# Performance work log

Measured on AMD Instinct MI355X. Metric: run time of the kernel, lower is better.

The kernel has to match this reference:

```python
import jax, jax.numpy as jnp
import numpy as np

EMBED_DIM = 1024
NUM_HEADS = 16
HEAD_DIM = EMBED_DIM // NUM_HEADS


def setup_inputs() -> dict:
    key = jax.random.key(0)
    ks = jax.random.split(key, 9)
    B, S, D = 2, 2048, EMBED_DIM
    scale = 1.0 / np.sqrt(D)
    x = jax.random.normal(ks[0], (B, S, D), dtype=jnp.float32)
    # Linear params (torch nn.Linear: y = x @ W.T + b); store W as [out, in]
    Wq = jax.random.normal(ks[1], (D, D), dtype=jnp.float32) * scale
    bq = jnp.zeros((D,), dtype=jnp.float32)
    Wk = jax.random.normal(ks[2], (D, D), dtype=jnp.float32) * scale
    bk = jnp.zeros((D,), dtype=jnp.float32)
    Wv = jax.random.normal(ks[3], (D, D), dtype=jnp.float32) * scale
    bv = jnp.zeros((D,), dtype=jnp.float32)
    Wo = jax.random.normal(ks[4], (D, D), dtype=jnp.float32) * scale
    bo = jnp.zeros((D,), dtype=jnp.float32)
    return {"x": x, "Wq": Wq, "bq": bq, "Wk": Wk, "bk": bk,
            "Wv": Wv, "bv": bv, "Wo": Wo, "bo": bo}


def reference(x, Wq, bq, Wk, bk, Wv, bv, Wo, bo):
    B, S, D = x.shape
    H, Hd = NUM_HEADS, HEAD_DIM
    scaling = Hd ** -0.5
    # projections (torch Linear: x @ W.T + b)
    q = (x @ Wq.T + bq).reshape(B, S, H, Hd).transpose(0, 2, 1, 3)  # [B,H,S,Hd]
    k = (x @ Wk.T + bk).reshape(B, S, H, Hd).transpose(0, 2, 1, 3)
    v = (x @ Wv.T + bv).reshape(B, S, H, Hd).transpose(0, 2, 1, 3)
    # full score matrix, as in the original (no flash tiling)
    scores = jnp.einsum('bhqd,bhkd->bhqk', q, k) * scaling  # [B,H,S,S]
    attn = jax.nn.softmax(scores, axis=-1)
    # dropout is identity in eval mode
    out = jnp.einsum('bhqk,bhkd->bhqd', attn, v)  # [B,H,S,Hd]
    out = out.transpose(0, 2, 1, 3).reshape(B, S, D)
    return out @ Wo.T + bo
```

## Files before the change

### kernel.cpp

```cpp
#include <hip/hip_runtime.h>
#include <stdint.h>

typedef unsigned short u16;
typedef short short8 __attribute__((ext_vector_type(8)));
typedef float f32x4 __attribute__((ext_vector_type(4)));

__device__ __forceinline__ u16 f2bf_fast(float f) {
  union { float f; uint32_t u; } x;
  x.f = f;
  return (u16)((x.u + 0x8000u) >> 16);
}

__device__ __forceinline__ uint32_t pack2bf(float lo, float hi) {
  union { float f; uint32_t u; } a, b;
  a.f = lo; b.f = hi;
  return __builtin_amdgcn_perm(b.u + 0x8000u, a.u + 0x8000u, 0x07060302u);
}

__device__ __forceinline__ float bf2f(uint32_t u) {
  union { uint32_t u; float f; } x;
  x.u = u << 16;
  return x.f;
}

__device__ __forceinline__ void gload_lds16(const void* g, void* l) {
  __builtin_amdgcn_global_load_lds(
      (const __attribute__((address_space(1))) void*)g,
      (__attribute__((address_space(3))) void*)l, 16, 0, 0);
}

__device__ __forceinline__ f32x4 mfma16(short8 a, short8 b, f32x4 c) {
  return __builtin_amdgcn_mfma_f32_16x16x32_bf16(a, b, c, 0, 0, 0);
}

__device__ __forceinline__ short8 ldfrag(const u16* base, int tile, int kc,
                                         int lane) {
  return *(const short8*)(base + ((((tile << 5) + kc) << 6) + lane) * 8);
}

#define QSCALE 0.18033688011112042f

__global__ void pack_all(const float* __restrict__ x, const float* __restrict__ wq,
                         const float* __restrict__ wk, const float* __restrict__ wv,
                         const float* __restrict__ wo, u16* __restrict__ xp,
                         u16* __restrict__ wp) {
  const int gi = blockIdx.x * 256 + threadIdx.x;
  const int lane = gi & 63;
  const int kc = (gi >> 6) & 31;
  const int rt = gi >> 11;
  const int col = kc * 32 + (lane >> 4) * 8;
  const float* src;
  int row;
  if (rt < 256) {
    src = x;
    row = rt * 16 + (lane & 15);
  } else {
    const int wti = rt - 256;
    const int widx = wti >> 6;
    src = (widx == 0) ? wq : (widx == 1) ? wk : (widx == 2) ? wv : wo;
    row = (wti & 63) * 16 + (lane & 15);
  }
  const float4* p = (const float4*)(src + (size_t)row * 1024 + col);
  const float4 v0 = p[0], v1 = p[1];
  uint4 o;
  o.x = pack2bf(v0.x, v0.y);
  o.y = pack2bf(v0.z, v0.w);
  o.z = pack2bf(v1.x, v1.y);
  o.w = pack2bf(v1.z, v1.w);
  u16* dst = (rt < 256) ? xp : wp;
  const int og = (rt < 256) ? gi : gi - 524288;
  ((uint4*)dst)[og] = o;
}

__global__ __launch_bounds__(256, 3) void proj_qkv(
    const u16* __restrict__ xp, const u16* __restrict__ wp,
    const float* __restrict__ bq, const float* __restrict__ bk,
    const float* __restrict__ bv, u16* __restrict__ qw, u16* __restrict__ kw,
    u16* __restrict__ vw) {
  const int wv2 = threadIdx.x >> 6;
  const int lane = threadIdx.x & 63;
  const int quad = lane >> 4, l15 = lane & 15;
  const int xcd = blockIdx.x & 7;
  const int bidx = blockIdx.x >> 3;
  const int xq = xcd >> 1, xh = xcd & 1;
  const bool isQK = bidx < 64;
  int at0, bt0, bm, bn;
  const u16 *Ap, *Bp;
  if (isQK) {
    const int q = bidx;
    bn = xh * 16 + (q & 15);
    bm = xq * 16 + (q >> 4) * 4 + wv2;
    Ap = xp; at0 = bm * 4;
    Bp = wp; bt0 = bn * 4;
  } else {
    const int v = bidx - 64;
    bn = xq * 16 + (v & 15);
    bm = xh * 8 + (v >> 4) * 4 + wv2;
    Ap = wp; at0 = 128 + bm * 4;
    Bp = xp; bt0 = bn * 4;
  }

  f32x4 acc[4][4] = {};
  short8 af[2][4], bf[2][4];
#pragma unroll
  for (int mt = 0; mt < 4; ++mt) af[0][mt] = ldfrag(Ap, at0 + mt, 0, lane);
#pragma unroll
  for (int nt = 0; nt < 4; ++nt) bf[0][nt] = ldfrag(Bp, bt0 + nt, 0, lane);

#pragma unroll 4
  for (int kc = 0; kc < 32; ++kc) {
    const int cur = kc & 1, nxt = cur ^ 1;
    if (kc < 31) {
#pragma unroll
      for (int mt = 0; mt < 4; ++mt)
        af[nxt][mt] = ldfrag(Ap, at0 + mt, kc + 1, lane);
#pragma unroll
      for (int nt = 0; nt < 4; ++nt)
        bf[nxt][nt] = ldfrag(Bp, bt0 + nt, kc + 1, lane);
    }
#pragma unroll
    for (int mt = 0; mt < 4; ++mt)
#pragma unroll
      for (int nt = 0; nt < 4; ++nt)
        acc[mt][nt] = mfma16(af[cur][mt], bf[cur][nt], acc[mt][nt]);
  }

#pragma unroll
  for (int nt = 0; nt < 4; ++nt) {
    const int n = bn * 64 + nt * 16 + l15;
#pragma unroll
    for (int mt = 0; mt < 4; ++mt)
#pragma unroll
      for (int r = 0; r < 4; ++r) {
        const int m = bm * 64 + mt * 16 + quad * 4 + r;
        const float a = acc[mt][nt][r];
        if (isQK) {
          const bool isQ = (bn < 16);
          const int nn = isQ ? n : n - 1024;
          const float v = isQ ? (a + bq[nn]) * QSCALE : a + bk[nn];
          u16* op = isQ ? qw : kw;
          const int b = m >> 11, s = m & 2047, hh = nn >> 6, d = nn & 63;
          op[((size_t)((b * 16 + hh) * 2048 + s)) * 64 + d] = f2bf_fast(v);
        } else {
          const float v = a + bv[m];
          const int b = n >> 11, s = n & 2047;
          vw[((size_t)(b * 1024 + m)) * 2048 + s] = f2bf_fast(v);
        }
      }
  }
}

__global__ __launch_bounds__(256) void attn_kernel(
    const u16* __restrict__ Q, const u16* __restrict__ Kt,
    const u16* __restrict__ Vt, u16* __restrict__ op0, u16* __restrict__ op1,
    float* __restrict__ lp) {
  __shared__ __align__(16) u16 Sm[16384];
  const int tid = threadIdx.x, lane = tid & 63, w = tid >> 6;
  const int quad = lane >> 4, l15 = lane & 15;
  const int qt = blockIdx.x;
  const int bh = blockIdx.y >> 1;
  const int ks = blockIdx.y & 1;
  const int sl = (l15 & 3) | ((l15 >> 1) & 4) | ((l15 << 1) & 8);

  const char* Qb = (const char*)(Q + ((size_t)bh * 2048 + qt * 128) * 64);
  const char* Kb = (const char*)(Kt + ((size_t)bh * 2048 + ks * 1024) * 64);
  const char* Vb = (const char*)(Vt + (size_t)bh * 64 * 2048 + ks * 1024);

  auto stageKV = [&](int kt, int b) {
    u16* Kl = Sm + b * 4096;
    u16* Vl = Sm + 8192 + b * 4096;
#pragma unroll
    for (int i = 0; i < 2; ++i) {
      const int G = (w * 2 + i) * 64 + lane;
      const int r = G >> 3, slw = G & 7;
      gload_lds16(Kb + (size_t)(kt * 64 + r) * 128 + ((slw ^ (r & 7)) * 16),
                  &Kl[G * 8]);
      gload_lds16(Vb + (size_t)r * 4096 + kt * 128 + ((slw ^ (r & 7)) * 16),
                  &Vl[G * 8]);
    }
  };

#pragma unroll
  for (int i = 0; i < 4; ++i) {
    const int G = (w * 4 + i) * 64 + lane;
    const int row = G >> 3, slw = G & 7;
    u16* qdst = (G < 512) ? (Sm + 4096) : (Sm + 12288);
    gload_lds16(Qb + (size_t)row * 128 + ((slw ^ (row & 7)) * 16),
                &qdst[(G & 511) * 8]);
  }
  stageKV(0, 0);
  __syncthreads();

  const u16* qreg = (w < 2) ? (Sm + 4096) : (Sm + 12288);
  const int qr0 = (w & 1) * 32;
  short8 aq[2][2];
#pragma unroll
  for (int mt = 0; mt < 2; ++mt)
#pragma unroll
    for (int kc = 0; kc < 2; ++kc)
      aq[mt][kc] = *(const short8*)&qreg[(qr0 + mt * 16 + l15) * 64 +
                                         (((kc * 4 + quad) ^ (l15 & 7)) * 8)];
  __syncthreads();

  f32x4 ot[4][2] = {};
  float lsum[2] = {};

  for (int kt = 0; kt < 16; ++kt) {
    const int buf = kt & 1;
    if (kt < 15) stageKV(kt + 1, buf ^ 1);
    const u16* Kl = Sm + buf * 4096;
    const u16* Vl = Sm + 8192 + buf * 4096;

    f32x4 st[2][4] = {};
#pragma unroll
    for (int kc = 0; kc < 2; ++kc)
#pragma unroll
      for (int ntk = 0; ntk < 4; ++ntk) {
        short8 kf = *(const short8*)&Kl[(ntk * 16 + sl) * 64 +
                                        (((kc * 4 + quad) ^ (sl & 7)) * 8)];
        st[0][ntk] = mfma16(kf, aq[0][kc], st[0][ntk]);
        st[1][ntk] = mfma16(kf, aq[1][kc], st[1][ntk]);
      }

    uint2 pp[2][4];
#pragma unroll
    for (int mt = 0; mt < 2; ++mt)
#pragma unroll
      for (int ntk = 0; ntk < 4; ++ntk) {
        const float e0 = __builtin_amdgcn_exp2f(st[mt][ntk][0]);
        const float e1 = __builtin_amdgcn_exp2f(st[mt][ntk][1]);
        const float e2 = __builtin_amdgcn_exp2f(st[mt][ntk][2]);
        const float e3 = __builtin_amdgcn_exp2f(st[mt][ntk][3]);
        lsum[mt] += (e0 + e1) + (e2 + e3);
        pp[mt][ntk].x = pack2bf(e0, e1);
        pp[mt][ntk].y = pack2bf(e2, e3);
      }

    short8 pf[2][2];
#pragma unroll
    for (int mt = 0; mt < 2; ++mt)
#pragma unroll
      for (int g = 0; g < 2; ++g) {
        const uint2 o0 = pp[mt][2 * g], o1 = pp[mt][2 * g + 1];
        const uint32_t x0l = __shfl_xor(o0.x, 32), x0h = __shfl_xor(o0.y, 32);
        const uint32_t x1l = __shfl_xor(o1.x, 32), x1h = __shfl_xor(o1.y, 32);
        union { uint32_t u[4]; short8 s; } f;
        if (quad < 2) {
          f.u[0] = o0.x; f.u[1] = o0.y; f.u[2] = x0l; f.u[3] = x0h;
        } else {
          f.u[0] = x1l; f.u[1] = x1h; f.u[2] = o1.x; f.u[3] = o1.y;
        }
        pf[mt][g] = f.s;
      }

#pragma unroll
    for (int g = 0; g < 2; ++g)
#pragma unroll
      for (int ntd = 0; ntd < 4; ++ntd) {
        short8 vf = *(const short8*)&Vl[(ntd * 16 + l15) * 64 +
                                        (((g * 4 + quad) ^ (l15 & 7)) * 8)];
        ot[ntd][0] = mfma16(vf, pf[0][g], ot[ntd][0]);
        ot[ntd][1] = mfma16(vf, pf[1][g], ot[ntd][1]);
      }
    if (kt < 15) __syncthreads();
  }

  const int b = bh >> 4, h = bh & 15;
  u16* op = ks ? op1 : op0;
#pragma unroll
  for (int mt = 0; mt < 2; ++mt) {
    float l = lsum[mt];
    l += __shfl_xor(l, 16);
    l += __shfl_xor(l, 32);
    const int srow = qt * 128 + w * 32 + mt * 16 + l15;
    if (quad == 0) lp[((size_t)(ks * 32 + bh)) * 2048 + srow] = l;
    const int rt = b * 128 + qt * 8 + w * 2 + mt;
#pragma unroll
    for (int ntd = 0; ntd < 4; ++ntd) {
      const int kc = h * 2 + (ntd >> 1);
      const int lnq = ((ntd & 1) * 2 + (quad >> 1)) & 3;
      const int j0 = (quad & 1) * 4;
      uint2 ov;
      ov.x = pack2bf(ot[ntd][mt][0], ot[ntd][mt][1]);
      ov.y = pack2bf(ot[ntd][mt][2], ot[ntd][mt][3]);
      *(uint2*)(op + ((size_t)((rt * 32 + kc) * 64 + lnq * 16 + l15)) * 8 + j0) = ov;
    }
  }
}

__global__ void attn_combine(const u16* __restrict__ op0,
                             const u16* __restrict__ op1,
                             const float* __restrict__ lp,
                             u16* __restrict__ awp) {
  const int g = blockIdx.x * 256 + threadIdx.x;
  const int ln = g & 63;
  const int kc = (g >> 6) & 31;
  const int rt = g >> 11;
  const int row = rt * 16 + (ln & 15);
  const int b = row >> 11, s = row & 2047;
  const int h = kc >> 1;
  const int lidx = (b * 16 + h) * 2048 + s;
  const float inv = __builtin_amdgcn_rcpf(lp[lidx] + lp[lidx + 65536]);
  const uint4 a0 = ((const uint4*)op0)[g];
  const uint4 a1 = ((const uint4*)op1)[g];
  uint4 o;
  o.x = pack2bf((bf2f(a0.x) + bf2f(a1.x)) * inv,
                (bf2f(a0.x >> 16) + bf2f(a1.x >> 16)) * inv);
  o.y = pack2bf((bf2f(a0.y) + bf2f(a1.y)) * inv,
                (bf2f(a0.y >> 16) + bf2f(a1.y >> 16)) * inv);
  o.z = pack2bf((bf2f(a0.z) + bf2f(a1.z)) * inv,
                (bf2f(a0.z >> 16) + bf2f(a1.z >> 16)) * inv);
  o.w = pack2bf((bf2f(a0.w) + bf2f(a1.w)) * inv,
                (bf2f(a0.w >> 16) + bf2f(a1.w >> 16)) * inv);
  ((uint4*)awp)[g] = o;
}

__global__ __launch_bounds__(256, 3) void out_proj(const u16* __restrict__ awp,
                                                   const u16* __restrict__ wp,
                                                   const float* __restrict__ bo,
                                                   float* __restrict__ out) {
  const int wv2 = threadIdx.x >> 6;
  const int lane = threadIdx.x & 63;
  const int quad = lane >> 4, l15 = lane & 15;
  const int xcd = blockIdx.x & 7;
  const int bidx = blockIdx.x >> 3;
  const int xq = xcd >> 1, xh = xcd & 1;
  const int bnn = xh * 16 + (bidx & 15);
  const int bm = xq * 16 + (bidx >> 4) * 4 + wv2;
  const int at0 = bm * 4, bt0 = 192 + bnn * 2;

  f32x4 acc[4][2] = {};
  short8 af[2][4], bf[2][2];
#pragma unroll
  for (int mt = 0; mt < 4; ++mt) af[0][mt] = ldfrag(awp, at0 + mt, 0, lane);
#pragma unroll
  for (int nt = 0; nt < 2; ++nt) bf[0][nt] = ldfrag(wp, bt0 + nt, 0, lane);

#pragma unroll 4
  for (int kc = 0; kc < 32; ++kc) {
    const int cur = kc & 1, nxt = cur ^ 1;
    if (kc < 31) {
#pragma unroll
      for (int mt = 0; mt < 4; ++mt)
        af[nxt][mt] = ldfrag(awp, at0 + mt, kc + 1, lane);
#pragma unroll
      for (int nt = 0; nt < 2; ++nt)
        bf[nxt][nt] = ldfrag(wp, bt0 + nt, kc + 1, lane);
    }
#pragma unroll
    for (int mt = 0; mt < 4; ++mt)
#pragma unroll
      for (int nt = 0; nt < 2; ++nt)
        acc[mt][nt] = mfma16(af[cur][mt], bf[cur][nt], acc[mt][nt]);
  }

#pragma unroll
  for (int nt = 0; nt < 2; ++nt) {
    const int n = bnn * 32 + nt * 16 + l15;
    const float bb = bo[n];
#pragma unroll
    for (int mt = 0; mt < 4; ++mt)
#pragma unroll
      for (int r = 0; r < 4; ++r) {
        const int m = bm * 64 + mt * 16 + quad * 4 + r;
        out[(size_t)m * 1024 + n] = acc[mt][nt][r] + bb;
      }
  }
}

extern "C" void kernel_launch(void* const* d_in, const int* in_sizes, int n_in,
                              void* d_out, int out_size, void* d_ws, size_t ws_size,
                              hipStream_t stream) {
  const float* x  = (const float*)d_in[0];
  const float* Wq = (const float*)d_in[1];
  const float* bq = (const float*)d_in[2];
  const float* Wk = (const float*)d_in[3];
  const float* bk = (const float*)d_in[4];
  const float* Wv = (const float*)d_in[5];
  const float* bv = (const float*)d_in[6];
  const float* Wo = (const float*)d_in[7];
  const float* bo = (const float*)d_in[8];

  const size_t M4 = (size_t)4 * 1024 * 1024;
  u16* xp  = (u16*)d_ws;
  u16* wp  = xp + M4;
  u16* qw  = wp + M4;
  u16* kw  = qw + M4;
  u16* vw  = kw + M4;
  u16* op1 = vw + M4;
  u16* awp = op1 + M4;
  float* lp = (float*)(awp + M4);
  u16* op0 = xp;

  pack_all<<<4096, 256, 0, stream>>>(x, Wq, Wk, Wv, Wo, xp, wp);

  proj_qkv<<<768, 256, 0, stream>>>(xp, wp, bq, bk, bv, qw, kw, vw);

  attn_kernel<<<dim3(16, 64), 256, 0, stream>>>(qw, kw, vw, op0, op1, lp);

  attn_combine<<<2048, 256, 0, stream>>>(op0, op1, lp, awp);

  out_proj<<<512, 256, 0, stream>>>(awp, wp, bo, (float*)d_out);
}
```

Before: 215.6 us.

## Write Q/K/V in MFMA fragment order and load attention operands directly from global

The QKV projection now writes Q, K and V straight into per-lane MFMA fragment-packed layouts, with the K row permutation baked in. The attention kernel drops its LDS staging, double buffering and barriers and reads fragments straight from global memory into registers, with the key loop unrolled by two. This removes LDS traffic and synchronisation, but K/V reuse across the four waves of a block now depends on L1/L2 caching. It also adds scattered stores in the projection epilogue and raises register pressure.

```diff
diff --git a/kernel.cpp b/kernel.cpp
--- a/kernel.cpp
+++ b/kernel.cpp
@@ -21,12 +21,6 @@
   union { uint32_t u; float f; } x;
   x.u = u << 16;
   return x.f;
-}
-
-__device__ __forceinline__ void gload_lds16(const void* g, void* l) {
-  __builtin_amdgcn_global_load_lds(
-      (const __attribute__((address_space(1))) void*)g,
-      (__attribute__((address_space(3))) void*)l, 16, 0, 0);
 }
 
 __device__ __forceinline__ f32x4 mfma16(short8 a, short8 b, f32x4 c) {
@@ -75,8 +69,8 @@
 __global__ __launch_bounds__(256, 3) void proj_qkv(
     const u16* __restrict__ xp, const u16* __restrict__ wp,
     const float* __restrict__ bq, const float* __restrict__ bk,
-    const float* __restrict__ bv, u16* __restrict__ qw, u16* __restrict__ kw,
-    u16* __restrict__ vw) {
+    const float* __restrict__ bv, u16* __restrict__ qp, u16* __restrict__ kp,
+    u16* __restrict__ vp) {
   const int wv2 = threadIdx.x >> 6;
   const int lane = threadIdx.x & 63;
   const int quad = lane >> 4, l15 = lane & 15;
@@ -137,89 +131,76 @@
         if (isQK) {
           const bool isQ = (bn < 16);
           const int nn = isQ ? n : n - 1024;
+          const int hh = nn >> 6, d = nn & 63;
+          const int b = m >> 11, s2 = m & 2047;
+          const int bh = b * 16 + hh;
           const float v = isQ ? (a + bq[nn]) * QSCALE : a + bk[nn];
-          u16* op = isQ ? qw : kw;
-          const int b = m >> 11, s = m & 2047, hh = nn >> 6, d = nn & 63;
-          op[((size_t)((b * 16 + hh) * 2048 + s)) * 64 + d] = f2bf_fast(v);
+          const int s4 = s2 & 15;
+          const int lp_ = isQ ? s4 : ((s4 & 3) | ((s4 >> 1) & 4) | ((s4 << 1) & 8));
+          u16* dst = isQ ? qp : kp;
+          dst[((size_t)bh * 256 + (s2 >> 4) * 2 + (d >> 5)) * 512 +
+              ((((d >> 3) & 3) * 16 + lp_) * 8) + (d & 7)] = f2bf_fast(v);
         } else {
+          const int hh = m >> 6, dd = m & 63;
+          const int b = n >> 11, s2 = n & 2047;
+          const int bh = b * 16 + hh;
           const float v = a + bv[m];
-          const int b = n >> 11, s = n & 2047;
-          vw[((size_t)(b * 1024 + m)) * 2048 + s] = f2bf_fast(v);
+          vp[((size_t)bh * 256 + (dd >> 4) * 64 + (s2 >> 5)) * 512 +
+             ((((s2 >> 3) & 3) * 16 + (dd & 15)) * 8) + (s2 & 7)] = f2bf_fast(v);
         }
       }
   }
 }
 
 __global__ __launch_bounds__(256) void attn_kernel(
-    const u16* __restrict__ Q, const u16* __restrict__ Kt,
-    const u16* __restrict__ Vt, u16* __restrict__ op0, u16* __restrict__ op1,
+    const u16* __restrict__ qp, const u16* __restrict__ kp,
+    const u16* __restrict__ vp, u16* __restrict__ op0, u16* __restrict__ op1,
     float* __restrict__ lp) {
-  __shared__ __align__(16) u16 Sm[16384];
   const int tid = threadIdx.x, lane = tid & 63, w = tid >> 6;
   const int quad = lane >> 4, l15 = lane & 15;
   const int qt = blockIdx.x;
   const int bh = blockIdx.y >> 1;
   const int ks = blockIdx.y & 1;
-  const int sl = (l15 & 3) | ((l15 >> 1) & 4) | ((l15 << 1) & 8);
-
-  const char* Qb = (const char*)(Q + ((size_t)bh * 2048 + qt * 128) * 64);
-  const char* Kb = (const char*)(Kt + ((size_t)bh * 2048 + ks * 1024) * 64);
-  const char* Vb = (const char*)(Vt + (size_t)bh * 64 * 2048 + ks * 1024);
-
-  auto stageKV = [&](int kt, int b) {
-    u16* Kl = Sm + b * 4096;
-    u16* Vl = Sm + 8192 + b * 4096;
-#pragma unroll
-    for (int i = 0; i < 2; ++i) {
-      const int G = (w * 2 + i) * 64 + lane;
-      const int r = G >> 3, slw = G & 7;
-      gload_lds16(Kb + (size_t)(kt * 64 + r) * 128 + ((slw ^ (r & 7)) * 16),
-                  &Kl[G * 8]);
-      gload_lds16(Vb + (size_t)r * 4096 + kt * 128 + ((slw ^ (r & 7)) * 16),
-                  &Vl[G * 8]);
-    }
-  };
-
-#pragma unroll
-  for (int i = 0; i < 4; ++i) {
-    const int G = (w * 4 + i) * 64 + lane;
-    const int row = G >> 3, slw = G & 7;
-    u16* qdst = (G < 512) ? (Sm + 4096) : (Sm + 12288);
-    gload_lds16(Qb + (size_t)row * 128 + ((slw ^ (row & 7)) * 16),
-                &qdst[(G & 511) * 8]);
-  }
-  stageKV(0, 0);
-  __syncthreads();
-
-  const u16* qreg = (w < 2) ? (Sm + 4096) : (Sm + 12288);
-  const int qr0 = (w & 1) * 32;
+
+  const u16* qb = qp + (size_t)bh * 131072;
+  const u16* kb = kp + (size_t)bh * 131072;
+  const u16* vb = vp + (size_t)bh * 131072;
+
   short8 aq[2][2];
 #pragma unroll
   for (int mt = 0; mt < 2; ++mt)
 #pragma unroll
     for (int kc = 0; kc < 2; ++kc)
-      aq[mt][kc] = *(const short8*)&qreg[(qr0 + mt * 16 + l15) * 64 +
-                                         (((kc * 4 + quad) ^ (l15 & 7)) * 8)];
-  __syncthreads();
+      aq[mt][kc] = *(const short8*)(qb +
+          ((((size_t)((qt * 4 + w) * 2 + mt) * 2 + kc) << 6) + lane) * 8);
 
   f32x4 ot[4][2] = {};
   float lsum[2] = {};
 
+#pragma unroll 2
   for (int kt = 0; kt < 16; ++kt) {
-    const int buf = kt & 1;
-    if (kt < 15) stageKV(kt + 1, buf ^ 1);
-    const u16* Kl = Sm + buf * 4096;
-    const u16* Vl = Sm + 8192 + buf * 4096;
+    short8 kf[4][2];
+#pragma unroll
+    for (int ntk = 0; ntk < 4; ++ntk)
+#pragma unroll
+      for (int kc = 0; kc < 2; ++kc)
+        kf[ntk][kc] = *(const short8*)(kb +
+            ((((size_t)(ks * 64 + kt * 4 + ntk) * 2 + kc) << 6) + lane) * 8);
+    short8 vf[4][2];
+#pragma unroll
+    for (int ntd = 0; ntd < 4; ++ntd)
+#pragma unroll
+      for (int g = 0; g < 2; ++g)
+        vf[ntd][g] = *(const short8*)(vb +
+            (((size_t)(ntd * 64 + ks * 32 + kt * 2 + g) << 6) + lane) * 8);
 
     f32x4 st[2][4] = {};
 #pragma unroll
     for (int kc = 0; kc < 2; ++kc)
 #pragma unroll
       for (int ntk = 0; ntk < 4; ++ntk) {
-        short8 kf = *(const short8*)&Kl[(ntk * 16 + sl) * 64 +
-                                        (((kc * 4 + quad) ^ (sl & 7)) * 8)];
-        st[0][ntk] = mfma16(kf, aq[0][kc], st[0][ntk]);
-        st[1][ntk] = mfma16(kf, aq[1][kc], st[1][ntk]);
+        st[0][ntk] = mfma16(kf[ntk][kc], aq[0][kc], st[0][ntk]);
+        st[1][ntk] = mfma16(kf[ntk][kc], aq[1][kc], st[1][ntk]);
       }
 
     uint2 pp[2][4];
@@ -257,12 +238,9 @@
     for (int g = 0; g < 2; ++g)
 #pragma unroll
       for (int ntd = 0; ntd < 4; ++ntd) {
-        short8 vf = *(const short8*)&Vl[(ntd * 16 + l15) * 64 +
-                                        (((g * 4 + quad) ^ (l15 & 7)) * 8)];
-        ot[ntd][0] = mfma16(vf, pf[0][g], ot[ntd][0]);
-        ot[ntd][1] = mfma16(vf, pf[1][g], ot[ntd][1]);
-      }
-    if (kt < 15) __syncthreads();
+        ot[ntd][0] = mfma16(vf[ntd][g], pf[0][g], ot[ntd][0]);
+        ot[ntd][1] = mfma16(vf[ntd][g], pf[1][g], ot[ntd][1]);
+      }
   }
 
   const int b = bh >> 4, h = bh & 15;
@@ -384,19 +362,19 @@
   const size_t M4 = (size_t)4 * 1024 * 1024;
   u16* xp  = (u16*)d_ws;
   u16* wp  = xp + M4;
-  u16* qw  = wp + M4;
-  u16* kw  = qw + M4;
-  u16* vw  = kw + M4;
-  u16* op1 = vw + M4;
+  u16* qp  = wp + M4;
+  u16* kp  = qp + M4;
+  u16* vp  = kp + M4;
+  u16* op1 = vp + M4;
   u16* awp = op1 + M4;
   float* lp = (float*)(awp + M4);
   u16* op0 = xp;
 
   pack_all<<<4096, 256, 0, stream>>>(x, Wq, Wk, Wv, Wo, xp, wp);
 
-  proj_qkv<<<768, 256, 0, stream>>>(xp, wp, bq, bk, bv, qw, kw, vw);
-
-  attn_kernel<<<dim3(16, 64), 256, 0, stream>>>(qw, kw, vw, op0, op1, lp);
+  proj_qkv<<<768, 256, 0, stream>>>(xp, wp, bq, bk, bv, qp, kp, vp);
+
+  attn_kernel<<<dim3(16, 64), 256, 0, stream>>>(qp, kp, vp, op0, op1, lp);
 
   attn_combine<<<2048, 256, 0, stream>>>(op0, op1, lp, awp);
 
```

New measurement: 292.2 us. 1.36x slower.
